# Optimization experiments

Hardware: AMD Instinct MI355X
Metric: run time of the kernel (lower is better)

The kernel has to match this reference:

```python
import jax, jax.numpy as jnp
from jax import lax
import numpy as np

DN = ('NCHW', 'OIHW', 'NCHW')

def conv(x, w, b, stride=1, groups=1):
    y = lax.conv_general_dilated(x, w, (stride, stride), 'SAME',
                                 feature_group_count=groups, dimension_numbers=DN)
    return y + b[None, :, None, None]

def sep_conv(x, dw, pw, pb):
    # depthwise 3x3 -> pointwise 1x1 -> ReLU (BN is frozen at identity)
    y = lax.conv_general_dilated(x, dw, (1, 1), 'SAME',
                                 feature_group_count=x.shape[1], dimension_numbers=DN)
    return jax.nn.relu(conv(y, pw, pb))

def up2(x):
    return jnp.repeat(jnp.repeat(x, 2, axis=2), 2, axis=3)

def down2(x):
    return lax.reduce_window(x, -jnp.inf, lax.max, (1, 1, 2, 2), (1, 1, 2, 2), 'VALID')

def fuse(w, *xs):
    # fast normalized fusion
    w = jax.nn.relu(w)
    w = w / (jnp.sum(w) + 1e-4)
    out = w[0] * xs[0]
    for i in range(1, len(xs)):
        out = out + w[i] * xs[i]
    return out

def bifpn_layer(ps, dw, pw, pb, fw2, fw3):
    p3, p4, p5, p6, p7 = ps
    p6t = sep_conv(fuse(fw2[0], p6, up2(p7)),  dw[0], pw[0], pb[0])
    p5t = sep_conv(fuse(fw2[1], p5, up2(p6t)), dw[1], pw[1], pb[1])
    p4t = sep_conv(fuse(fw2[2], p4, up2(p5t)), dw[2], pw[2], pb[2])
    p3o = sep_conv(fuse(fw2[3], p3, up2(p4t)), dw[3], pw[3], pb[3])
    p4o = sep_conv(fuse(fw3[0], p4, p4t, down2(p3o)), dw[4], pw[4], pb[4])
    p5o = sep_conv(fuse(fw3[1], p5, p5t, down2(p4o)), dw[5], pw[5], pb[5])
    p6o = sep_conv(fuse(fw3[2], p6, p6t, down2(p5o)), dw[6], pw[6], pb[6])
    p7o = sep_conv(fuse(fw2[4], p7, down2(p6o)),      dw[7], pw[7], pb[7])
    return [p3o, p4o, p5o, p6o, p7o]

def make_anchors(img_size):
    # RetinaNet-style anchors: pyramid levels 3..7, 3 scales x 3 ratios
    ratios = np.array([0.5, 1.0, 2.0])
    scales = 2.0 ** (np.arange(3) / 3.0)
    boxes_all = []
    for lvl in range(3, 8):
        stride = 2 ** lvl
        size = 2 ** (lvl + 2)
        fs = img_size // stride
        ws = (size * scales[None, :] / np.sqrt(ratios)[:, None]).reshape(-1)  # [9]
        hs = (size * scales[None, :] * np.sqrt(ratios)[:, None]).reshape(-1)
        ctr = (np.arange(fs) + 0.5) * stride
        gy, gx = np.meshgrid(ctr, ctr, indexing='ij')
        centers = np.stack([gx, gy], -1).reshape(-1, 1, 2)      # [HW,1,2] (x,y)
        wh = np.stack([ws, hs], -1)[None]                       # [1,9,2]
        boxes = np.concatenate([centers - wh / 2, centers + wh / 2], -1).reshape(-1, 4)
        boxes_all.append(boxes)
    return jnp.asarray(np.concatenate(boxes_all, 0), jnp.float32)

def run_head(p, tw, tb, ow, ob, out_ch):
    x = p
    for i in range(tw.shape[0]):
        x = jax.nn.relu(conv(x, tw[i], tb[i]))
    y = conv(x, ow, ob)                                  # [B, 9*out_ch, H, W]
    B, _, H, W = y.shape
    return y.transpose(0, 2, 3, 1).reshape(B, H * W * 9, out_ch)

def setup_inputs() -> dict:
    key = jax.random.key(0)
    ks = iter(jax.random.split(key, 64))
    B, W, NC, ST, D = 4, 88, 90, 3, 4
    chans = [40, 80, 112, 192, 320]
    hw = [64, 32, 16, 8, 4]
    inp = {}
    for i, (c, h) in enumerate(zip(chans, hw)):
        inp[f'c{i+3}'] = jax.random.normal(next(ks), (B, c, h, h), jnp.float32)
        inp[f'lat_w{i+3}'] = jax.random.normal(next(ks), (W, c, 1, 1), jnp.float32) * 0.05
        inp[f'lat_b{i+3}'] = jnp.zeros((W,), jnp.float32)
    inp['bif_dw'] = jax.random.normal(next(ks), (ST, 8, W, 1, 3, 3), jnp.float32) * 0.1
    inp['bif_pw'] = jax.random.normal(next(ks), (ST, 8, W, W, 1, 1), jnp.float32) * 0.05
    inp['bif_pb'] = jnp.zeros((ST, 8, W), jnp.float32)
    inp['bif_fw2'] = jnp.ones((ST, 5, 2), jnp.float32)
    inp['bif_fw3'] = jnp.ones((ST, 3, 3), jnp.float32)
    inp['reg_tw'] = jax.random.normal(next(ks), (D, W, W, 3, 3), jnp.float32) * 0.03
    inp['reg_tb'] = jnp.zeros((D, W), jnp.float32)
    inp['reg_ow'] = jax.random.normal(next(ks), (36, W, 3, 3), jnp.float32) * 0.01
    inp['reg_ob'] = jnp.zeros((36,), jnp.float32)
    inp['cls_tw'] = jax.random.normal(next(ks), (D, W, W, 3, 3), jnp.float32) * 0.03
    inp['cls_tb'] = jnp.zeros((D, W), jnp.float32)
    inp['cls_ow'] = jax.random.normal(next(ks), (9 * NC, W, 3, 3), jnp.float32) * 0.01
    inp['cls_ob'] = jnp.full((9 * NC,), -np.log((1.0 - 0.01) / 0.01), jnp.float32)
    inp['img_size'] = 512
    return inp

def reference(c3, c4, c5, c6, c7,
              lat_w3, lat_b3, lat_w4, lat_b4, lat_w5, lat_b5,
              lat_w6, lat_b6, lat_w7, lat_b7,
              bif_dw, bif_pw, bif_pb, bif_fw2, bif_fw3,
              reg_tw, reg_tb, reg_ow, reg_ob,
              cls_tw, cls_tb, cls_ow, cls_ob,
              img_size):
    num_classes = cls_ow.shape[0] // 9
    ps = [conv(c3, lat_w3, lat_b3), conv(c4, lat_w4, lat_b4), conv(c5, lat_w5, lat_b5),
          conv(c6, lat_w6, lat_b6), conv(c7, lat_w7, lat_b7)]
    for s in range(bif_dw.shape[0]):
        ps = bifpn_layer(ps, bif_dw[s], bif_pw[s], bif_pb[s], bif_fw2[s], bif_fw3[s])
    regression = jnp.concatenate([run_head(p, reg_tw, reg_tb, reg_ow, reg_ob, 4) for p in ps], axis=1)
    classification = jnp.concatenate(
        [jax.nn.sigmoid(run_head(p, cls_tw, cls_tb, cls_ow, cls_ob, num_classes)) for p in ps], axis=1)
    anchors = make_anchors(int(img_size))
    return classification, regression, anchors
```

## Files before the change

kernel.cpp:

```cpp
#include <hip/hip_runtime.h>
#include <math.h>

#define TPB 256
static inline int cdiv(int a, int b) { return (a + b - 1) / b; }

typedef __attribute__((ext_vector_type(8))) short short8;
typedef __attribute__((ext_vector_type(4))) float floatx4;

__device__ __forceinline__ float bf2f(ushort u) {
    union { unsigned int u; float f; } v; v.u = ((unsigned int)u) << 16; return v.f;
}
__device__ __forceinline__ ushort f2bf(float f) {
    union { float f; unsigned int u; } v; v.f = f;
    unsigned int r = (v.u + 0x7FFFu + ((v.u >> 16) & 1u)) >> 16;
    return (ushort)r;
}

#define CONC_ROWS 21824
__device__ __forceinline__ void lvl_of(int row, int& lvl, int& base) {
    lvl = 0; base = 0;
    if (row >= 16384) { lvl = 1; base = 16384; }
    if (row >= 20480) { lvl = 2; base = 20480; }
    if (row >= 21504) { lvl = 3; base = 21504; }
    if (row >= 21760) { lvl = 4; base = 21760; }
}
__constant__ int LOFFc[5] = {0, 36864, 46080, 48384, 48960};
__constant__ int MLVc[5]  = {16384, 4096, 1024, 256, 64};

__global__ void pack3_k(const float* __restrict__ w, ushort* __restrict__ Bp,
                        int Ntot, int CO, int total) {
    int idx = blockIdx.x * blockDim.x + threadIdx.x;
    if (idx >= total) return;
    int j = idx & 7; int t = idx >> 3;
    int n = t % Ntot; t /= Ntot;
    int g = t & 3; t >>= 2;
    int ks = t % 3; int tap = t / 3;
    int ci = ks * 32 + g * 8 + j;
    float v = (ci < 88 && n < CO) ? w[((size_t)n * 88 + ci) * 9 + tap] : 0.f;
    Bp[idx] = f2bf(v);
}

__global__ void pack_tw8_k(const float* __restrict__ rw, const float* __restrict__ cw,
                           ushort* __restrict__ Bp) {
    int idx = blockIdx.x * blockDim.x + threadIdx.x;
    if (idx >= 8 * 82944) return;
    int i = idx / 82944; int r = idx - i * 82944;
    const float* w = (i < 4) ? rw + (size_t)i * 69696 : cw + (size_t)(i - 4) * 69696;
    int j = r & 7; int t = r >> 3;
    int n = t % 96; t /= 96;
    int g = t & 3; t >>= 2;
    int ks = t % 3; int tap = t / 3;
    int ci = ks * 32 + g * 8 + j;
    float v = (ci < 88 && n < 88) ? w[((size_t)n * 88 + ci) * 9 + tap] : 0.f;
    Bp[idx] = f2bf(v);
}

__global__ void pack_pw_all_k(const float* __restrict__ pw, ushort* __restrict__ Bp,
                              int total) {
    int idx = blockIdx.x * blockDim.x + threadIdx.x;
    if (idx >= total) return;
    int cid = idx / 9216; int r = idx - cid * 9216;
    int j = r & 7; int t = r >> 3;
    int n = t % 96; t /= 96;
    int g = t & 3; int ks = t >> 2;
    int ci = ks * 32 + g * 8 + j;
    float v = (ci < 88 && n < 88) ? pw[(size_t)cid * 7744 + n * 88 + ci] : 0.f;
    Bp[idx] = f2bf(v);
}

__global__ void pack_lat_k(const float* __restrict__ w3, const float* __restrict__ w4,
                           const float* __restrict__ w5, const float* __restrict__ w6,
                           const float* __restrict__ w7, ushort* __restrict__ Bp) {
    int idx = blockIdx.x * blockDim.x + threadIdx.x;
    if (idx >= 76800) return;
    int l, off;
    if (idx < 6144)       { l = 0; off = 0; }
    else if (idx < 15360) { l = 1; off = 6144; }
    else if (idx < 27648) { l = 2; off = 15360; }
    else if (idx < 46080) { l = 3; off = 27648; }
    else                  { l = 4; off = 46080; }
    const float* w = l == 0 ? w3 : l == 1 ? w4 : l == 2 ? w5 : l == 3 ? w6 : w7;
    const int cins[5] = {40, 80, 112, 192, 320};
    int Cin = cins[l];
    int r = idx - off;
    int j = r & 7; int t = r >> 3;
    int n = t % 96; t /= 96;
    int g = t & 3; int ks = t >> 2;
    int ci = ks * 32 + g * 8 + j;
    float v = (ci < Cin && n < 88) ? w[(size_t)n * Cin + ci] : 0.f;
    Bp[idx] = f2bf(v);
}

__global__ __launch_bounds__(256)
void lateral_mfma_k(const float* __restrict__ x, const ushort* __restrict__ Bp,
                    const float* __restrict__ bias, ushort* __restrict__ out,
                    int Cin, int KS, int logHH) {
    __shared__ ushort As[64 * 40];
    int tid = threadIdx.x;
    int m0 = blockIdx.x * 64;
    int lane = tid & 63, l15 = lane & 15, g = (lane >> 4) & 3;
    int wave = tid >> 6, wm = wave & 1, wn = wave >> 1;
    floatx4 acc[2][3];
#pragma unroll
    for (int a = 0; a < 2; ++a)
#pragma unroll
        for (int b = 0; b < 3; ++b) acc[a][b] = (floatx4){0.f, 0.f, 0.f, 0.f};
    const short8* Bq = (const short8*)Bp;

    int p = m0 + lane;
    int n = p >> logHH, pp = p & ((1 << logHH) - 1);
    const float* xp = x + (((size_t)n * Cin) << logHH) + pp;

    for (int ks = 0; ks < KS; ++ks) {
        __syncthreads();
#pragma unroll
        for (int it = 0; it < 8; ++it) {
            int ciL = (tid >> 6) + it * 4;
            int ci = ks * 32 + ciL;
            float v = (ci < Cin) ? xp[(size_t)ci << logHH] : 0.f;
            As[lane * 40 + ciL] = f2bf(v);
        }
        __syncthreads();
        short8 a0 = *(const short8*)(&As[(wm * 32 + l15) * 40 + g * 8]);
        short8 a1 = *(const short8*)(&As[(wm * 32 + 16 + l15) * 40 + g * 8]);
        int bbase = (ks * 4 + g) * 96 + wn * 48 + l15;
#pragma unroll
        for (int nf = 0; nf < 3; ++nf) {
            short8 b = Bq[bbase + nf * 16];
            acc[0][nf] = __builtin_amdgcn_mfma_f32_16x16x32_bf16(a0, b, acc[0][nf], 0, 0, 0);
            acc[1][nf] = __builtin_amdgcn_mfma_f32_16x16x32_bf16(a1, b, acc[1][nf], 0, 0, 0);
        }
    }
    float bc[3];
#pragma unroll
    for (int nf = 0; nf < 3; ++nf) {
        int c = wn * 48 + nf * 16 + l15;
        bc[nf] = (c < 88) ? bias[c] : 0.f;
    }
#pragma unroll
    for (int mf = 0; mf < 2; ++mf)
#pragma unroll
        for (int r = 0; r < 4; ++r) {
            int pl = m0 + wm * 32 + mf * 16 + g * 4 + r;
#pragma unroll
            for (int nf = 0; nf < 3; ++nf) {
                int c = wn * 48 + nf * 16 + l15;
                out[(size_t)pl * 96 + c] = f2bf(acc[mf][nf][r] + bc[nf]);
            }
        }
}

template <int MODE>
__global__ __launch_bounds__(256, 2)
void sepconv_k(const ushort* __restrict__ a, const ushort* __restrict__ bsrc,
               const ushort* __restrict__ csrc, const float* __restrict__ fw,
               const float* __restrict__ dww, const ushort* __restrict__ Bp,
               const float* __restrict__ pbias, ushort* __restrict__ out,
               int logW) {
    __shared__ ushort Fs[195 * 104];
    __shared__ ushort Ds[64 * 104];
    __shared__ ushort Dwb[108 * 8];
    int tid = threadIdx.x;
    int W = 1 << logW, HH = W * W, log2HH = 2 * logW;
    int Mlv = 4 * HH;
    int HB = W + 1;
    int RS = 64 + 2 * HB;
    int pl0 = blockIdx.x * 64;
    float w0 = fmaxf(fw[0], 0.f), w1 = fmaxf(fw[1], 0.f);
    float w2 = (MODE == 2) ? fmaxf(fw[2], 0.f) : 0.f;
    float inv = 1.f / (w0 + w1 + w2 + 1e-4f);
    float w0i = w0 * inv, w1i = w1 * inv, w2i = w2 * inv;

    if (tid < 13) *(uint4*)(&Fs[194 * 104 + tid * 8]) = (uint4){0u, 0u, 0u, 0u};
    for (int i = tid; i < 108; i += 256) {
        int cg = i / 9, tap = i - cg * 9;
        ushort tmp[8];
#pragma unroll
        for (int j = 0; j < 8; ++j) {
            int c = cg * 8 + j;
            tmp[j] = (c < 88) ? f2bf(dww[c * 9 + tap]) : (ushort)0;
        }
        *(uint4*)(&Dwb[i * 8]) = *(uint4*)tmp;
    }
    for (int i = tid; i < RS * 12; i += 256) {
        int row = i / 12, cg = i - row * 12;
        int pl = pl0 - HB + row;
        uint4 res = {0u, 0u, 0u, 0u};
        if (pl >= 0 && pl < Mlv) {
            int n = pl >> log2HH, pp = pl & (HH - 1);
            int y = pp >> logW, x = pp & (W - 1);
            uint4 av = *(const uint4*)(a + (size_t)pl * 96 + cg * 8);
            const ushort* au = (const ushort*)&av;
            float f[8];
            if (MODE == 0) {
                int Wh = W >> 1;
                int bp = (n << (log2HH - 2)) + (y >> 1) * Wh + (x >> 1);
                uint4 bv = *(const uint4*)(bsrc + (size_t)bp * 96 + cg * 8);
                const ushort* bu = (const ushort*)&bv;
#pragma unroll
                for (int j = 0; j < 8; ++j)
                    f[j] = w0i * bf2f(au[j]) + w1i * bf2f(bu[j]);
            } else {
                int W2 = W << 1;
                const ushort* q = (MODE == 1 ? bsrc : csrc) +
                    ((size_t)((n << (log2HH + 2)) + (2 * y) * W2 + 2 * x)) * 96 + cg * 8;
                uint4 q0 = *(const uint4*)(q);
                uint4 q1 = *(const uint4*)(q + 96);
                uint4 q2 = *(const uint4*)(q + (size_t)W2 * 96);
                uint4 q3 = *(const uint4*)(q + (size_t)W2 * 96 + 96);
                const ushort* u0 = (const ushort*)&q0; const ushort* u1 = (const ushort*)&q1;
                const ushort* u2 = (const ushort*)&q2; const ushort* u3 = (const ushort*)&q3;
                if (MODE == 1) {
#pragma unroll
                    for (int j = 0; j < 8; ++j) {
                        float m = fmaxf(fmaxf(bf2f(u0[j]), bf2f(u1[j])),
                                        fmaxf(bf2f(u2[j]), bf2f(u3[j])));
                        f[j] = w0i * bf2f(au[j]) + w1i * m;
                    }
                } else {
                    uint4 b2v = *(const uint4*)(bsrc + (size_t)pl * 96 + cg * 8);
                    const ushort* b2u = (const ushort*)&b2v;
#pragma unroll
                    for (int j = 0; j < 8; ++j) {
                        float m = fmaxf(fmaxf(bf2f(u0[j]), bf2f(u1[j])),
                                        fmaxf(bf2f(u2[j]), bf2f(u3[j])));
                        f[j] = w0i * bf2f(au[j]) + w1i * bf2f(b2u[j]) + w2i * m;
                    }
                }
            }
            ushort tmp[8];
#pragma unroll
            for (int j = 0; j < 8; ++j) tmp[j] = f2bf(f[j]);
            res = *(uint4*)tmp;
        }
        *(uint4*)(&Fs[row * 104 + cg * 8]) = res;
    }
    __syncthreads();
    for (int i = tid; i < 768; i += 256) {
        int row = i / 12, cg = i - row * 12;
        int pl = pl0 + row;
        int pp = pl & (HH - 1);
        int y = pp >> logW, x = pp & (W - 1);
        float acc8[8] = {0.f, 0.f, 0.f, 0.f, 0.f, 0.f, 0.f, 0.f};
        if (cg < 11) {
#pragma unroll
            for (int tap = 0; tap < 9; ++tap) {
                int dy = tap / 3 - 1, dx = tap % 3 - 1;
                int sy = y + dy, sx = x + dx;
                bool pred = ((unsigned)sy < (unsigned)W) && ((unsigned)sx < (unsigned)W);
                int rsel = pred ? (row + HB + dy * W + dx) : 194;
                short8 fv = *(const short8*)(&Fs[rsel * 104 + cg * 8]);
                short8 wv = *(const short8*)(&Dwb[(cg * 9 + tap) * 8]);
#pragma unroll
                for (int j = 0; j < 8; ++j)
                    acc8[j] = fmaf(bf2f((ushort)fv[j]), bf2f((ushort)wv[j]), acc8[j]);
            }
        }
        ushort tmp[8];
#pragma unroll
        for (int j = 0; j < 8; ++j) tmp[j] = f2bf(acc8[j]);
        *(uint4*)(&Ds[row * 104 + cg * 8]) = *(uint4*)tmp;
    }
    __syncthreads();
    int lane = tid & 63, l15 = lane & 15, g = (lane >> 4) & 3;
    int wave = tid >> 6, wm = wave & 1, wn = wave >> 1;
    floatx4 acc[2][3];
#pragma unroll
    for (int aa = 0; aa < 2; ++aa)
#pragma unroll
        for (int bb = 0; bb < 3; ++bb) acc[aa][bb] = (floatx4){0.f, 0.f, 0.f, 0.f};
    const short8* Bq = (const short8*)Bp;
#pragma unroll
    for (int ks = 0; ks < 3; ++ks) {
        int k = ks * 32 + g * 8;
        short8 a0 = *(const short8*)(&Ds[(wm * 32 + l15) * 104 + k]);
        short8 a1 = *(const short8*)(&Ds[(wm * 32 + 16 + l15) * 104 + k]);
        int bbase = (ks * 4 + g) * 96 + wn * 48 + l15;
#pragma unroll
        for (int nf = 0; nf < 3; ++nf) {
            short8 b = Bq[bbase + nf * 16];
            acc[0][nf] = __builtin_amdgcn_mfma_f32_16x16x32_bf16(a0, b, acc[0][nf], 0, 0, 0);
            acc[1][nf] = __builtin_amdgcn_mfma_f32_16x16x32_bf16(a1, b, acc[1][nf], 0, 0, 0);
        }
    }
    float bc[3];
#pragma unroll
    for (int nf = 0; nf < 3; ++nf) {
        int c = wn * 48 + nf * 16 + l15;
        bc[nf] = (c < 88) ? pbias[c] : 0.f;
    }
#pragma unroll
    for (int mf = 0; mf < 2; ++mf)
#pragma unroll
        for (int r = 0; r < 4; ++r) {
            int pl = pl0 + wm * 32 + mf * 16 + g * 4 + r;
#pragma unroll
            for (int nf = 0; nf < 3; ++nf) {
                int c = wn * 48 + nf * 16 + l15;
                out[(size_t)pl * 96 + c] = f2bf(fmaxf(acc[mf][nf][r] + bc[nf], 0.f));
            }
        }
}

__global__ __launch_bounds__(256, 2)
void tower_halo_k(const ushort* __restrict__ inR, const ushort* __restrict__ inC,
                  const ushort* __restrict__ BpR, const ushort* __restrict__ BpC,
                  const float* __restrict__ bR, const float* __restrict__ bC,
                  ushort* __restrict__ outR, ushort* __restrict__ outC) {
    __shared__ ushort As[259 * 104];
    int head = blockIdx.y;
    const ushort* in = head ? inC : inR;
    const short8* Bq = (const short8*)(head ? BpC : BpR);
    const float* bias = head ? bC : bR;
    ushort* out = head ? outC : outR;
    int tid = threadIdx.x;
    int m0 = blockIdx.x * 128;
    int lvl, base; lvl_of(m0, lvl, base);
    int logW = 6 - lvl, W = 1 << logW, HH = W * W, log2HH = 2 * logW;
    int Mlv = MLVc[lvl];
    int HB = W + 1;
    int RS = 128 + 2 * HB;
    if (tid < 13) *(uint4*)(&As[258 * 104 + tid * 8]) = (uint4){0u, 0u, 0u, 0u};
    for (int i = tid; i < RS * 12; i += 256) {
        int row = i / 12, cg = i - row * 12;
        int pl = m0 - base - HB + row;
        uint4 v = {0u, 0u, 0u, 0u};
        if (pl >= 0 && pl < Mlv)
            v = *(const uint4*)(in + (size_t)(base + pl) * 96 + cg * 8);
        *(uint4*)(&As[row * 104 + cg * 8]) = v;
    }
    __syncthreads();
    int lane = tid & 63, l15 = lane & 15, g = (lane >> 4) & 3;
    int wave = tid >> 6, wm = wave & 1, wn = wave >> 1;
    int pl0 = m0 - base;
    int rL[4], xm[4], ym[4]; bool vm[4];
#pragma unroll
    for (int mf = 0; mf < 4; ++mf) {
        rL[mf] = wm * 64 + mf * 16 + l15;
        int pl = pl0 + rL[mf];
        vm[mf] = pl < Mlv;
        int pp = pl & (HH - 1);
        ym[mf] = pp >> logW; xm[mf] = pp & (W - 1);
    }
    floatx4 acc[4][3];
#pragma unroll
    for (int aa = 0; aa < 4; ++aa)
#pragma unroll
        for (int bb = 0; bb < 3; ++bb) acc[aa][bb] = (floatx4){0.f, 0.f, 0.f, 0.f};
#pragma unroll
    for (int tap = 0; tap < 9; ++tap) {
        int dy = tap / 3 - 1, dx = tap % 3 - 1;
        int rs[4];
#pragma unroll
        for (int mf = 0; mf < 4; ++mf) {
            bool pred = vm[mf] && ((unsigned)(ym[mf] + dy) < (unsigned)W) &&
                        ((unsigned)(xm[mf] + dx) < (unsigned)W);
            rs[mf] = pred ? (HB + rL[mf] + dy * W + dx) : 258;
        }
#pragma unroll
        for (int ks = 0; ks < 3; ++ks) {
            short8 bfr[3];
            int bbase = ((tap * 3 + ks) * 4 + g) * 96 + wn * 48 + l15;
#pragma unroll
            for (int nf = 0; nf < 3; ++nf) bfr[nf] = Bq[bbase + nf * 16];
#pragma unroll
            for (int mf = 0; mf < 4; ++mf) {
                short8 af = *(const short8*)(&As[rs[mf] * 104 + ks * 32 + g * 8]);
#pragma unroll
                for (int nf = 0; nf < 3; ++nf)
                    acc[mf][nf] = __builtin_amdgcn_mfma_f32_16x16x32_bf16(af, bfr[nf], acc[mf][nf], 0, 0, 0);
            }
        }
    }
    float bc[3];
#pragma unroll
    for (int nf = 0; nf < 3; ++nf) {
        int c = wn * 48 + nf * 16 + l15;
        bc[nf] = (c < 88) ? bias[c] : 0.f;
    }
#pragma unroll
    for (int mf = 0; mf < 4; ++mf)
#pragma unroll
        for (int r = 0; r < 4; ++r) {
            int pl = pl0 + wm * 64 + mf * 16 + g * 4 + r;
            if (pl >= Mlv) continue;
#pragma unroll
            for (int nf = 0; nf < 3; ++nf) {
                int c = wn * 48 + nf * 16 + l15;
                out[(size_t)(base + pl) * 96 + c] = f2bf(fmaxf(acc[mf][nf][r] + bc[nf], 0.f));
            }
        }
}

template <int OC, bool SIG>
__global__ __launch_bounds__(256, 2)
void head_halo_k(const ushort* __restrict__ in, const ushort* __restrict__ Bp,
                 const float* __restrict__ bias, float* __restrict__ outb,
                 int Ntot, int C9) {
    __shared__ ushort As[259 * 104];
    int tid = threadIdx.x;
    int m0 = blockIdx.x * 128;
    int n0b = blockIdx.y * 96;
    int lvl, base; lvl_of(m0, lvl, base);
    int logW = 6 - lvl, W = 1 << logW, HH = W * W, log2HH = 2 * logW;
    int Mlv = MLVc[lvl];
    int HB = W + 1;
    int RS = 128 + 2 * HB;
    if (tid < 13) *(uint4*)(&As[258 * 104 + tid * 8]) = (uint4){0u, 0u, 0u, 0u};
    for (int i = tid; i < RS * 12; i += 256) {
        int row = i / 12, cg = i - row * 12;
        int pl = m0 - base - HB + row;
        uint4 v = {0u, 0u, 0u, 0u};
        if (pl >= 0 && pl < Mlv)
            v = *(const uint4*)(in + (size_t)(base + pl) * 96 + cg * 8);
        *(uint4*)(&As[row * 104 + cg * 8]) = v;
    }
    __syncthreads();
    int lane = tid & 63, l15 = lane & 15, g = (lane >> 4) & 3;
    int wave = tid >> 6, wm = wave & 1, wn = wave >> 1;
    int pl0 = m0 - base;
    int rL[4], xm[4], ym[4]; bool vm[4];
#pragma unroll
    for (int mf = 0; mf < 4; ++mf) {
        rL[mf] = wm * 64 + mf * 16 + l15;
        int pl = pl0 + rL[mf];
        vm[mf] = pl < Mlv;
        int pp = pl & (HH - 1);
        ym[mf] = pp >> logW; xm[mf] = pp & (W - 1);
    }
    floatx4 acc[4][3];
#pragma unroll
    for (int aa = 0; aa < 4; ++aa)
#pragma unroll
        for (int bb = 0; bb < 3; ++bb) acc[aa][bb] = (floatx4){0.f, 0.f, 0.f, 0.f};
    const short8* Bq = (const short8*)Bp;
#pragma unroll
    for (int tap = 0; tap < 9; ++tap) {
        int dy = tap / 3 - 1, dx = tap % 3 - 1;
        int rs[4];
#pragma unroll
        for (int mf = 0; mf < 4; ++mf) {
            bool pred = vm[mf] && ((unsigned)(ym[mf] + dy) < (unsigned)W) &&
                        ((unsigned)(xm[mf] + dx) < (unsigned)W);
            rs[mf] = pred ? (HB + rL[mf] + dy * W + dx) : 258;
        }
#pragma unroll
        for (int ks = 0; ks < 3; ++ks) {
            short8 bfr[3];
            int bbase = ((tap * 3 + ks) * 4 + g) * Ntot + n0b + wn * 48 + l15;
#pragma unroll
            for (int nf = 0; nf < 3; ++nf) bfr[nf] = Bq[bbase + nf * 16];
#pragma unroll
            for (int mf = 0; mf < 4; ++mf) {
                short8 af = *(const short8*)(&As[rs[mf] * 104 + ks * 32 + g * 8]);
#pragma unroll
                for (int nf = 0; nf < 3; ++nf)
                    acc[mf][nf] = __builtin_amdgcn_mfma_f32_16x16x32_bf16(af, bfr[nf], acc[mf][nf], 0, 0, 0);
            }
        }
    }
#pragma unroll
    for (int nf = 0; nf < 3; ++nf) {
        int c = n0b + wn * 48 + nf * 16 + l15;
        if (c >= C9) continue;
        float bcv = bias[c];
        int a = c / OC, kk = c - a * OC;
#pragma unroll
        for (int mf = 0; mf < 4; ++mf)
#pragma unroll
            for (int r = 0; r < 4; ++r) {
                int pl = pl0 + wm * 64 + mf * 16 + g * 4 + r;
                if (pl >= Mlv) continue;
                int n = pl >> log2HH, pp = pl & (HH - 1);
                float v = acc[mf][nf][r] + bcv;
                if (SIG) v = 1.f / (1.f + expf(-v));
                outb[((size_t)n * 49104 + LOFFc[lvl] + (size_t)pp * 9 + a) * OC + kk] = v;
            }
    }
}

__global__ void anchors_k(float* __restrict__ out) {
    int idx = blockIdx.x * blockDim.x + threadIdx.x;
    if (idx >= 49104) return;
    const int offs[6] = {0, 36864, 46080, 48384, 48960, 49104};
    int l = 0;
    while (idx >= offs[l + 1]) ++l;
    int j = idx - offs[l];
    int a = j % 9;
    int p = j / 9;
    int fs = 64 >> l;
    int stride = 8 << l;
    float size = (float)(32 << l);
    int ix = p % fs, iy = p / fs;
    float cx = (ix + 0.5f) * (float)stride;
    float cy = (iy + 0.5f) * (float)stride;
    const float scl[3] = {1.0f, 1.2599210498948732f, 1.5874010519681994f};
    const float sqr[3] = {0.7071067811865476f, 1.0f, 1.4142135623730951f};
    int r = a / 3, s = a % 3;
    float w = size * scl[s] / sqr[r];
    float h = size * scl[s] * sqr[r];
    float* o = out + (size_t)idx * 4;
    o[0] = cx - 0.5f * w;
    o[1] = cy - 0.5f * h;
    o[2] = cx + 0.5f * w;
    o[3] = cy + 0.5f * h;
}


extern "C" void kernel_launch(void* const* d_in, const int* in_sizes, int n_in,
                              void* d_out, int out_size, void* d_ws, size_t ws_size,
                              hipStream_t stream) {
    const float* c_in[5]  = {(const float*)d_in[0],  (const float*)d_in[3],
                             (const float*)d_in[6],  (const float*)d_in[9],
                             (const float*)d_in[12]};
    const float* lat_w[5] = {(const float*)d_in[1],  (const float*)d_in[4],
                             (const float*)d_in[7],  (const float*)d_in[10],
                             (const float*)d_in[13]};
    const float* lat_b[5] = {(const float*)d_in[2],  (const float*)d_in[5],
                             (const float*)d_in[8],  (const float*)d_in[11],
                             (const float*)d_in[14]};
    const float* bif_dw  = (const float*)d_in[15];
    const float* bif_pw  = (const float*)d_in[16];
    const float* bif_pb  = (const float*)d_in[17];
    const float* bif_fw2 = (const float*)d_in[18];
    const float* bif_fw3 = (const float*)d_in[19];
    const float* reg_tw  = (const float*)d_in[20];
    const float* reg_tb  = (const float*)d_in[21];
    const float* reg_ow  = (const float*)d_in[22];
    const float* reg_ob  = (const float*)d_in[23];
    const float* cls_tw  = (const float*)d_in[24];
    const float* cls_tb  = (const float*)d_in[25];
    const float* cls_ow  = (const float*)d_in[26];
    const float* cls_ob  = (const float*)d_in[27];

    const int CINL[5] = {40, 80, 112, 192, 320};
    const int KSL[5]  = {2, 3, 4, 6, 10};
    const int LATO[5] = {0, 6144, 15360, 27648, 46080};
    const int ROFF[5] = {0, 16384, 20480, 21504, 21760};
    const int ML[5]   = {16384, 4096, 1024, 256, 64};
    const size_t CONC = (size_t)CONC_ROWS * 96;

    ushort* ws = (ushort*)d_ws;
    size_t off = 0;
    ushort* CA = ws + off; off += CONC;
    ushort* CB = ws + off; off += CONC;
    ushort* T4 = ws + off; off += (size_t)4096 * 96;
    ushort* T5 = ws + off; off += (size_t)1024 * 96;
    ushort* T6 = ws + off; off += (size_t)256 * 96;
    ushort* HXR0 = ws + off; off += CONC;
    ushort* HXR1 = ws + off; off += CONC;
    ushort* HXC0 = ws + off; off += CONC;
    ushort* HXC1 = ws + off; off += CONC;
    ushort* BP_PW  = ws + off; off += (size_t)24 * 9216;
    ushort* BP_TW  = ws + off; off += (size_t)8 * 82944;
    ushort* BP_RO  = ws + off; off += (size_t)82944;
    ushort* BP_CO  = ws + off; off += (size_t)746496;
    ushort* BP_LAT = ws + off; off += (size_t)76800;
    (void)ws_size; (void)n_in; (void)in_sizes; (void)out_size;

    pack_pw_all_k<<<cdiv(24 * 9216, TPB), TPB, 0, stream>>>(bif_pw, BP_PW, 24 * 9216);
    pack_tw8_k<<<cdiv(8 * 82944, TPB), TPB, 0, stream>>>(reg_tw, cls_tw, BP_TW);
    pack3_k<<<cdiv(82944, TPB), TPB, 0, stream>>>(reg_ow, BP_RO, 96, 36, 82944);
    pack3_k<<<cdiv(746496, TPB), TPB, 0, stream>>>(cls_ow, BP_CO, 864, 810, 746496);
    pack_lat_k<<<cdiv(76800, TPB), TPB, 0, stream>>>(
        lat_w[0], lat_w[1], lat_w[2], lat_w[3], lat_w[4], BP_LAT);

    float* cls_base = (float*)d_out;
    float* reg_base = cls_base + (size_t)4 * 49104 * 90;
    float* anc_base = reg_base + (size_t)4 * 49104 * 4;
    anchors_k<<<cdiv(49104, TPB), TPB, 0, stream>>>(anc_base);

    for (int l = 0; l < 5; ++l) {
        int logHH = 2 * (6 - l);
        lateral_mfma_k<<<ML[l] / 64, 256, 0, stream>>>(
            c_in[l], BP_LAT + LATO[l], lat_b[l], CA + (size_t)ROFF[l] * 96,
            CINL[l], KSL[l], logHH);
    }

    ushort* cur = CA; ushort* nxt = CB;
    for (int s = 0; s < 3; ++s) {
        const float* dws = bif_dw + (size_t)s * 8 * 792;
        const float* pbs = bif_pb + (size_t)s * 8 * 88;
        const float* f2  = bif_fw2 + (size_t)s * 10;
        const float* f3  = bif_fw3 + (size_t)s * 9;
        auto LP = [&](ushort* buf, int l) { return buf + (size_t)ROFF[l] * 96; };
        auto BPW = [&](int ci) { return BP_PW + (size_t)(s * 8 + ci) * 9216; };

        sepconv_k<0><<<ML[3] / 64, 256, 0, stream>>>(
            LP(cur, 3), LP(cur, 4), nullptr, f2 + 0, dws + 0 * 792, BPW(0), pbs + 0 * 88, T6, 3);
        sepconv_k<0><<<ML[2] / 64, 256, 0, stream>>>(
            LP(cur, 2), T6, nullptr, f2 + 2, dws + 1 * 792, BPW(1), pbs + 1 * 88, T5, 4);
        sepconv_k<0><<<ML[1] / 64, 256, 0, stream>>>(
            LP(cur, 1), T5, nullptr, f2 + 4, dws + 2 * 792, BPW(2), pbs + 2 * 88, T4, 5);
        sepconv_k<0><<<ML[0] / 64, 256, 0, stream>>>(
            LP(cur, 0), T4, nullptr, f2 + 6, dws + 3 * 792, BPW(3), pbs + 3 * 88, LP(nxt, 0), 6);
        sepconv_k<2><<<ML[1] / 64, 256, 0, stream>>>(
            LP(cur, 1), T4, LP(nxt, 0), f3 + 0, dws + 4 * 792, BPW(4), pbs + 4 * 88, LP(nxt, 1), 5);
        sepconv_k<2><<<ML[2] / 64, 256, 0, stream>>>(
            LP(cur, 2), T5, LP(nxt, 1), f3 + 3, dws + 5 * 792, BPW(5), pbs + 5 * 88, LP(nxt, 2), 4);
        sepconv_k<2><<<ML[3] / 64, 256, 0, stream>>>(
            LP(cur, 3), T6, LP(nxt, 2), f3 + 6, dws + 6 * 792, BPW(6), pbs + 6 * 88, LP(nxt, 3), 3);
        sepconv_k<1><<<ML[4] / 64, 256, 0, stream>>>(
            LP(cur, 4), LP(nxt, 3), nullptr, f2 + 8, dws + 7 * 792, BPW(7), pbs + 7 * 88, LP(nxt, 4), 2);

        ushort* tp = cur; cur = nxt; nxt = tp;
    }

    const int GB = 171;
    ushort* hxr[2] = {HXR0, HXR1};
    ushort* hxc[2] = {HXC0, HXC1};
    const ushort* xr = cur;
    const ushort* xc = cur;
    for (int i = 0; i < 4; ++i) {
        tower_halo_k<<<dim3(GB, 2), 256, 0, stream>>>(
            xr, xc, BP_TW + (size_t)i * 82944, BP_TW + (size_t)(4 + i) * 82944,
            reg_tb + i * 88, cls_tb + i * 88, hxr[i & 1], hxc[i & 1]);
        xr = hxr[i & 1]; xc = hxc[i & 1];
    }
    head_halo_k<4, false><<<dim3(GB, 1), 256, 0, stream>>>(
        xr, BP_RO, reg_ob, reg_base, 96, 36);
    head_halo_k<90, true><<<dim3(GB, 9), 256, 0, stream>>>(
        xc, BP_CO, cls_ob, cls_base, 864, 810);
}
```

Before: 726.7 us.

## Replace LDS halo staging with direct global loads in tower and head convs

The tower and head 3x3 conv kernels no longer stage a halo tile in shared memory. Each lane now reads its A fragments straight from global memory (L1/L2), and out-of-bounds taps point at a small zero buffer that anchors_k clears. The M tile drops from 128 to 64 rows, doubling the block count, and the launch-bounds occupancy hint is removed. This removes the LDS fill and the barrier at the cost of repeated global reads for the 9 taps and less B-fragment reuse per load.

```diff
diff --git a/kernel.cpp b/kernel.cpp
--- a/kernel.cpp
+++ b/kernel.cpp
@@ -25,7 +25,6 @@
     if (row >= 21760) { lvl = 4; base = 21760; }
 }
 __constant__ int LOFFc[5] = {0, 36864, 46080, 48384, 48960};
-__constant__ int MLVc[5]  = {16384, 4096, 1024, 256, 64};
 
 __global__ void pack3_k(const float* __restrict__ w, ushort* __restrict__ Bp,
                         int Ntot, int CO, int total) {
@@ -302,73 +301,60 @@
         }
 }
 
-__global__ __launch_bounds__(256, 2)
-void tower_halo_k(const ushort* __restrict__ inR, const ushort* __restrict__ inC,
-                  const ushort* __restrict__ BpR, const ushort* __restrict__ BpC,
-                  const float* __restrict__ bR, const float* __restrict__ bC,
-                  ushort* __restrict__ outR, ushort* __restrict__ outC) {
-    __shared__ ushort As[259 * 104];
+__global__ __launch_bounds__(256)
+void tower_direct_k(const ushort* __restrict__ inR, const ushort* __restrict__ inC,
+                    const ushort* __restrict__ BpR, const ushort* __restrict__ BpC,
+                    const float* __restrict__ bR, const float* __restrict__ bC,
+                    ushort* __restrict__ outR, ushort* __restrict__ outC,
+                    const ushort* __restrict__ zb) {
     int head = blockIdx.y;
     const ushort* in = head ? inC : inR;
     const short8* Bq = (const short8*)(head ? BpC : BpR);
     const float* bias = head ? bC : bR;
     ushort* out = head ? outC : outR;
     int tid = threadIdx.x;
-    int m0 = blockIdx.x * 128;
+    int m0 = blockIdx.x * 64;
     int lvl, base; lvl_of(m0, lvl, base);
-    int logW = 6 - lvl, W = 1 << logW, HH = W * W, log2HH = 2 * logW;
-    int Mlv = MLVc[lvl];
-    int HB = W + 1;
-    int RS = 128 + 2 * HB;
-    if (tid < 13) *(uint4*)(&As[258 * 104 + tid * 8]) = (uint4){0u, 0u, 0u, 0u};
-    for (int i = tid; i < RS * 12; i += 256) {
-        int row = i / 12, cg = i - row * 12;
-        int pl = m0 - base - HB + row;
-        uint4 v = {0u, 0u, 0u, 0u};
-        if (pl >= 0 && pl < Mlv)
-            v = *(const uint4*)(in + (size_t)(base + pl) * 96 + cg * 8);
-        *(uint4*)(&As[row * 104 + cg * 8]) = v;
-    }
-    __syncthreads();
+    int logW = 6 - lvl, W = 1 << logW, HH = W * W;
+    int pl0 = m0 - base;
     int lane = tid & 63, l15 = lane & 15, g = (lane >> 4) & 3;
     int wave = tid >> 6, wm = wave & 1, wn = wave >> 1;
-    int pl0 = m0 - base;
-    int rL[4], xm[4], ym[4]; bool vm[4];
-#pragma unroll
-    for (int mf = 0; mf < 4; ++mf) {
-        rL[mf] = wm * 64 + mf * 16 + l15;
-        int pl = pl0 + rL[mf];
-        vm[mf] = pl < Mlv;
+    int ym[2], xm[2];
+    const ushort* pbase[2];
+#pragma unroll
+    for (int mf = 0; mf < 2; ++mf) {
+        int pl = pl0 + wm * 32 + mf * 16 + l15;
         int pp = pl & (HH - 1);
         ym[mf] = pp >> logW; xm[mf] = pp & (W - 1);
-    }
-    floatx4 acc[4][3];
-#pragma unroll
-    for (int aa = 0; aa < 4; ++aa)
+        pbase[mf] = in + (size_t)(base + pl) * 96 + g * 8;
+    }
+    const ushort* zbg = zb + g * 8;
+    floatx4 acc[2][3];
+#pragma unroll
+    for (int aa = 0; aa < 2; ++aa)
 #pragma unroll
         for (int bb = 0; bb < 3; ++bb) acc[aa][bb] = (floatx4){0.f, 0.f, 0.f, 0.f};
 #pragma unroll
     for (int tap = 0; tap < 9; ++tap) {
-        int dy = tap / 3 - 1, dx = tap % 3 - 1;
-        int rs[4];
-#pragma unroll
-        for (int mf = 0; mf < 4; ++mf) {
-            bool pred = vm[mf] && ((unsigned)(ym[mf] + dy) < (unsigned)W) &&
+        const int dy = tap / 3 - 1, dx = tap % 3 - 1;
+        int off96 = (dy * W + dx) * 96;
+        const ushort* ap[2];
+#pragma unroll
+        for (int mf = 0; mf < 2; ++mf) {
+            bool pred = ((unsigned)(ym[mf] + dy) < (unsigned)W) &&
                         ((unsigned)(xm[mf] + dx) < (unsigned)W);
-            rs[mf] = pred ? (HB + rL[mf] + dy * W + dx) : 258;
+            ap[mf] = pred ? (pbase[mf] + off96) : zbg;
         }
 #pragma unroll
         for (int ks = 0; ks < 3; ++ks) {
-            short8 bfr[3];
+            short8 a0 = *(const short8*)(ap[0] + ks * 32);
+            short8 a1 = *(const short8*)(ap[1] + ks * 32);
             int bbase = ((tap * 3 + ks) * 4 + g) * 96 + wn * 48 + l15;
 #pragma unroll
-            for (int nf = 0; nf < 3; ++nf) bfr[nf] = Bq[bbase + nf * 16];
-#pragma unroll
-            for (int mf = 0; mf < 4; ++mf) {
-                short8 af = *(const short8*)(&As[rs[mf] * 104 + ks * 32 + g * 8]);
-#pragma unroll
-                for (int nf = 0; nf < 3; ++nf)
-                    acc[mf][nf] = __builtin_amdgcn_mfma_f32_16x16x32_bf16(af, bfr[nf], acc[mf][nf], 0, 0, 0);
+            for (int nf = 0; nf < 3; ++nf) {
+                short8 b = Bq[bbase + nf * 16];
+                acc[0][nf] = __builtin_amdgcn_mfma_f32_16x16x32_bf16(a0, b, acc[0][nf], 0, 0, 0);
+                acc[1][nf] = __builtin_amdgcn_mfma_f32_16x16x32_bf16(a1, b, acc[1][nf], 0, 0, 0);
             }
         }
     }
@@ -379,11 +365,10 @@
         bc[nf] = (c < 88) ? bias[c] : 0.f;
     }
 #pragma unroll
-    for (int mf = 0; mf < 4; ++mf)
+    for (int mf = 0; mf < 2; ++mf)
 #pragma unroll
         for (int r = 0; r < 4; ++r) {
-            int pl = pl0 + wm * 64 + mf * 16 + g * 4 + r;
-            if (pl >= Mlv) continue;
+            int pl = pl0 + wm * 32 + mf * 16 + g * 4 + r;
 #pragma unroll
             for (int nf = 0; nf < 3; ++nf) {
                 int c = wn * 48 + nf * 16 + l15;
@@ -393,69 +378,55 @@
 }
 
 template <int OC, bool SIG>
-__global__ __launch_bounds__(256, 2)
-void head_halo_k(const ushort* __restrict__ in, const ushort* __restrict__ Bp,
-                 const float* __restrict__ bias, float* __restrict__ outb,
-                 int Ntot, int C9) {
-    __shared__ ushort As[259 * 104];
+__global__ __launch_bounds__(256)
+void head_direct_k(const ushort* __restrict__ in, const ushort* __restrict__ Bp,
+                   const float* __restrict__ bias, float* __restrict__ outb,
+                   int Ntot, int C9, const ushort* __restrict__ zb) {
     int tid = threadIdx.x;
-    int m0 = blockIdx.x * 128;
+    int m0 = blockIdx.x * 64;
     int n0b = blockIdx.y * 96;
     int lvl, base; lvl_of(m0, lvl, base);
     int logW = 6 - lvl, W = 1 << logW, HH = W * W, log2HH = 2 * logW;
-    int Mlv = MLVc[lvl];
-    int HB = W + 1;
-    int RS = 128 + 2 * HB;
-    if (tid < 13) *(uint4*)(&As[258 * 104 + tid * 8]) = (uint4){0u, 0u, 0u, 0u};
-    for (int i = tid; i < RS * 12; i += 256) {
-        int row = i / 12, cg = i - row * 12;
-        int pl = m0 - base - HB + row;
-        uint4 v = {0u, 0u, 0u, 0u};
-        if (pl >= 0 && pl < Mlv)
-            v = *(const uint4*)(in + (size_t)(base + pl) * 96 + cg * 8);
-        *(uint4*)(&As[row * 104 + cg * 8]) = v;
-    }
-    __syncthreads();
+    int pl0 = m0 - base;
     int lane = tid & 63, l15 = lane & 15, g = (lane >> 4) & 3;
     int wave = tid >> 6, wm = wave & 1, wn = wave >> 1;
-    int pl0 = m0 - base;
-    int rL[4], xm[4], ym[4]; bool vm[4];
-#pragma unroll
-    for (int mf = 0; mf < 4; ++mf) {
-        rL[mf] = wm * 64 + mf * 16 + l15;
-        int pl = pl0 + rL[mf];
-        vm[mf] = pl < Mlv;
+    int ym[2], xm[2];
+    const ushort* pbase[2];
+#pragma unroll
+    for (int mf = 0; mf < 2; ++mf) {
+        int pl = pl0 + wm * 32 + mf * 16 + l15;
         int pp = pl & (HH - 1);
         ym[mf] = pp >> logW; xm[mf] = pp & (W - 1);
-    }
-    floatx4 acc[4][3];
-#pragma unroll
-    for (int aa = 0; aa < 4; ++aa)
+        pbase[mf] = in + (size_t)(base + pl) * 96 + g * 8;
+    }
+    const ushort* zbg = zb + g * 8;
+    floatx4 acc[2][3];
+#pragma unroll
+    for (int aa = 0; aa < 2; ++aa)
 #pragma unroll
         for (int bb = 0; bb < 3; ++bb) acc[aa][bb] = (floatx4){0.f, 0.f, 0.f, 0.f};
     const short8* Bq = (const short8*)Bp;
 #pragma unroll
     for (int tap = 0; tap < 9; ++tap) {
-        int dy = tap / 3 - 1, dx = tap % 3 - 1;
-        int rs[4];
-#pragma unroll
-        for (int mf = 0; mf < 4; ++mf) {
-            bool pred = vm[mf] && ((unsigned)(ym[mf] + dy) < (unsigned)W) &&
+        const int dy = tap / 3 - 1, dx = tap % 3 - 1;
+        int off96 = (dy * W + dx) * 96;
+        const ushort* ap[2];
+#pragma unroll
+        for (int mf = 0; mf < 2; ++mf) {
+            bool pred = ((unsigned)(ym[mf] + dy) < (unsigned)W) &&
                         ((unsigned)(xm[mf] + dx) < (unsigned)W);
-            rs[mf] = pred ? (HB + rL[mf] + dy * W + dx) : 258;
+            ap[mf] = pred ? (pbase[mf] + off96) : zbg;
         }
 #pragma unroll
         for (int ks = 0; ks < 3; ++ks) {
-            short8 bfr[3];
+            short8 a0 = *(const short8*)(ap[0] + ks * 32);
+            short8 a1 = *(const short8*)(ap[1] + ks * 32);
             int bbase = ((tap * 3 + ks) * 4 + g) * Ntot + n0b + wn * 48 + l15;
 #pragma unroll
-            for (int nf = 0; nf < 3; ++nf) bfr[nf] = Bq[bbase + nf * 16];
-#pragma unroll
-            for (int mf = 0; mf < 4; ++mf) {
-                short8 af = *(const short8*)(&As[rs[mf] * 104 + ks * 32 + g * 8]);
-#pragma unroll
-                for (int nf = 0; nf < 3; ++nf)
-                    acc[mf][nf] = __builtin_amdgcn_mfma_f32_16x16x32_bf16(af, bfr[nf], acc[mf][nf], 0, 0, 0);
+            for (int nf = 0; nf < 3; ++nf) {
+                short8 b = Bq[bbase + nf * 16];
+                acc[0][nf] = __builtin_amdgcn_mfma_f32_16x16x32_bf16(a0, b, acc[0][nf], 0, 0, 0);
+                acc[1][nf] = __builtin_amdgcn_mfma_f32_16x16x32_bf16(a1, b, acc[1][nf], 0, 0, 0);
             }
         }
     }
@@ -466,11 +437,10 @@
         float bcv = bias[c];
         int a = c / OC, kk = c - a * OC;
 #pragma unroll
-        for (int mf = 0; mf < 4; ++mf)
+        for (int mf = 0; mf < 2; ++mf)
 #pragma unroll
             for (int r = 0; r < 4; ++r) {
-                int pl = pl0 + wm * 64 + mf * 16 + g * 4 + r;
-                if (pl >= Mlv) continue;
+                int pl = pl0 + wm * 32 + mf * 16 + g * 4 + r;
                 int n = pl >> log2HH, pp = pl & (HH - 1);
                 float v = acc[mf][nf][r] + bcv;
                 if (SIG) v = 1.f / (1.f + expf(-v));
@@ -479,8 +449,9 @@
     }
 }
 
-__global__ void anchors_k(float* __restrict__ out) {
+__global__ void anchors_k(float* __restrict__ out, ushort* __restrict__ zb) {
     int idx = blockIdx.x * blockDim.x + threadIdx.x;
+    if (idx < 48) ((unsigned int*)zb)[idx] = 0u;
     if (idx >= 49104) return;
     const int offs[6] = {0, 36864, 46080, 48384, 48960, 49104};
     int l = 0;
@@ -556,6 +527,7 @@
     ushort* BP_RO  = ws + off; off += (size_t)82944;
     ushort* BP_CO  = ws + off; off += (size_t)746496;
     ushort* BP_LAT = ws + off; off += (size_t)76800;
+    ushort* ZB     = ws + off; off += 96;
     (void)ws_size; (void)n_in; (void)in_sizes; (void)out_size;
 
     pack_pw_all_k<<<cdiv(24 * 9216, TPB), TPB, 0, stream>>>(bif_pw, BP_PW, 24 * 9216);
@@ -568,7 +540,7 @@
     float* cls_base = (float*)d_out;
     float* reg_base = cls_base + (size_t)4 * 49104 * 90;
     float* anc_base = reg_base + (size_t)4 * 49104 * 4;
-    anchors_k<<<cdiv(49104, TPB), TPB, 0, stream>>>(anc_base);
+    anchors_k<<<cdiv(49104, TPB), TPB, 0, stream>>>(anc_base, ZB);
 
     for (int l = 0; l < 5; ++l) {
         int logHH = 2 * (6 - l);
@@ -606,19 +578,19 @@
         ushort* tp = cur; cur = nxt; nxt = tp;
     }
 
-    const int GB = 171;
+    const int GB = CONC_ROWS / 64;
     ushort* hxr[2] = {HXR0, HXR1};
     ushort* hxc[2] = {HXC0, HXC1};
     const ushort* xr = cur;
     const ushort* xc = cur;
     for (int i = 0; i < 4; ++i) {
-        tower_halo_k<<<dim3(GB, 2), 256, 0, stream>>>(
+        tower_direct_k<<<dim3(GB, 2), 256, 0, stream>>>(
             xr, xc, BP_TW + (size_t)i * 82944, BP_TW + (size_t)(4 + i) * 82944,
-            reg_tb + i * 88, cls_tb + i * 88, hxr[i & 1], hxc[i & 1]);
+            reg_tb + i * 88, cls_tb + i * 88, hxr[i & 1], hxc[i & 1], ZB);
         xr = hxr[i & 1]; xc = hxc[i & 1];
     }
-    head_halo_k<4, false><<<dim3(GB, 1), 256, 0, stream>>>(
-        xr, BP_RO, reg_ob, reg_base, 96, 36);
-    head_halo_k<90, true><<<dim3(GB, 9), 256, 0, stream>>>(
-        xc, BP_CO, cls_ob, cls_base, 864, 810);
-}
+    head_direct_k<4, false><<<dim3(GB, 1), 256, 0, stream>>>(
+        xr, BP_RO, reg_ob, reg_base, 96, 36, ZB);
+    head_direct_k<90, true><<<dim3(GB, 9), 256, 0, stream>>>(
+        xc, BP_CO, cls_ob, cls_base, 864, 810, ZB);
+}
```

Measured after the change: 688.2 us. -5.3%, faster.
